# Performance work log

Hardware: AMD Instinct MI355X
Metric: run time of the kernel (lower is better)

## Reference

```python
import jax, jax.numpy as jnp
import numpy as np

L = 8          # number of QTT cores = log2(init_reso)
RESO = 256     # init_reso
MAX_RANK = 256
N_SAMPLES = 4096


def _qtt_ranks(L, max_rank):
    return [min(8 ** k, 8 ** (L - k), max_rank) for k in range(L + 1)]


def setup_inputs() -> dict:
    key = jax.random.key(0)
    ranks = _qtt_ranks(L, MAX_RANK)
    keys = jax.random.split(key, L + 1)
    inp = {}
    for l in range(L):
        shape = (ranks[l], 8, ranks[l + 1])
        scale = (shape[0] * shape[1]) ** -0.5  # keep chain products O(1)
        inp[f"core{l}"] = jax.random.normal(keys[l], shape, dtype=jnp.float32) * scale
    inp["coords_xyz"] = jax.random.randint(keys[L], (N_SAMPLES, 3), 0, RESO)
    return inp


def _coords_to_qtt(coords_xyz, num_cores):
    # coords_xyz: (N, 3) int. Per core l (most-significant bit first):
    # c_l = 4*bit_x + 2*bit_y + bit_z in [0, 8)  -> shape (L, N)
    x, y, z = coords_xyz[:, 0], coords_xyz[:, 1], coords_xyz[:, 2]
    shifts = jnp.arange(num_cores - 1, -1, -1)[:, None]  # (L, 1)
    bx = (x[None, :] >> shifts) & 1
    by = (y[None, :] >> shifts) & 1
    bz = (z[None, :] >> shifts) & 1
    return 4 * bx + 2 * by + bz


def _sample_tt(cores, coords):
    # cores[l]: (r_l, 8, r_{l+1}); coords: (L, N)
    # v starts as first core slice: (N, r_1)  (r_0 == 1)
    v = cores[0][0, coords[0], :]
    for l in range(1, len(cores)):
        # gathered slice: (r_l, N, r_{l+1}) -> (N, r_l, r_{l+1})
        g = jnp.transpose(cores[l][:, coords[l], :], (1, 0, 2))
        v = jnp.einsum('nr,nrs->ns', v, g)
    return v[:, 0]  # r_L == 1 -> (N,)


def reference(core0, core1, core2, core3, core4, core5, core6, core7, coords_xyz):
    cores = [core0, core1, core2, core3, core4, core5, core6, core7]
    coords = _coords_to_qtt(coords_xyz, len(cores))
    return _sample_tt(cores, coords)
```

## Files before the change

### kernel.cpp

```cpp
#include <hip/hip_runtime.h>


typedef unsigned int u32;

__device__ __forceinline__ void async_load16(const float* g, float* l) {
    __builtin_amdgcn_global_load_lds(
        (const __attribute__((address_space(1))) u32*)g,
        (__attribute__((address_space(3))) u32*)l, 16, 0, 0);
}
__device__ __forceinline__ void fma4(float4& c, float a, const float4& b) {
    c.x = fmaf(a, b.x, c.x); c.y = fmaf(a, b.y, c.y);
    c.z = fmaf(a, b.z, c.z); c.w = fmaf(a, b.w, c.w);
}
__device__ __forceinline__ int digit_of(int x, int y, int z, int sh) {
    return 4*((x>>sh)&1) + 2*((y>>sh)&1) + ((z>>sh)&1);
}

__global__ __launch_bounds__(256, 4) void prep_kernel(
    const float* __restrict__ C4, const float* __restrict__ C5,
    const float* __restrict__ C6, const float* __restrict__ C7,
    float* __restrict__ T, float* __restrict__ C4t)
{
    const int t = threadIdx.x;
    const int bx = blockIdx.x;

    if (bx < 64) {
        __shared__ float S6s[8][64];
        const int d5 = bx >> 3, d6 = bx & 7;
#pragma unroll
        for (int j = 0; j < 2; ++j) {
            const int idx = t + 256*j, d7 = idx >> 6, s = idx & 63;
            float acc = 0.f;
#pragma unroll
            for (int jj = 0; jj < 8; ++jj)
                acc = fmaf(C6[s*64 + d6*8 + jj], C7[jj*8 + d7], acc);
            S6s[d7][s] = acc;
        }
        __syncthreads();
        float4 creg[16];
#pragma unroll
        for (int s4 = 0; s4 < 16; ++s4)
            creg[s4] = *(const float4*)(C5 + (size_t)t*512 + d5*64 + s4*4);
#pragma unroll 1
        for (int d7 = 0; d7 < 8; ++d7) {
            float acc = 0.f;
#pragma unroll
            for (int s4 = 0; s4 < 16; ++s4) {
                const float4 a = creg[s4];
                const float4 b = *(const float4*)&S6s[d7][s4*4];
                acc = fmaf(a.x, b.x, acc); acc = fmaf(a.y, b.y, acc);
                acc = fmaf(a.z, b.z, acc); acc = fmaf(a.w, b.w, acc);
            }
            T[(size_t)((d5*8 + d6)*8 + d7)*256 + t] = acc;
        }
    } else {
        const int cb = bx - 64;
        const int d4 = cb >> 2, s5q = cb & 3;
#pragma unroll 8
        for (int j = 0; j < 64; ++j) {
            const int s5 = s5q*64 + j;
            C4t[(size_t)d4*65536 + (size_t)s5*256 + t] =
                C4[(size_t)t*2048 + d4*256 + s5];
        }
    }
}

__device__ __forceinline__ void kgemm16(
    const float* __restrict__ Cd, int rowStride,
    const float (*As)[260], float* BsF,
    float* __restrict__ outP, int rowBase, int mulLo,
    int ln, int wv)
{
    const int kbase = wv * 64;
    float4 acc[16];
#pragma unroll
    for (int r = 0; r < 16; ++r) acc[r] = make_float4(0,0,0,0);

#pragma unroll 1
    for (int s = 0; s < 16; ++s) {
        if (s < 15) {
            const int nb = (s + 1) & 1;
            const int ko = kbase + (s + 1) * 4;
#pragma unroll
            for (int j = 0; j < 4; ++j)
                async_load16(Cd + (size_t)(ko + j)*rowStride + ln*4,
                             BsF + wv*2048 + nb*1024 + j*256 + ln*4);
            asm volatile("s_waitcnt vmcnt(4)" ::: "memory");
        } else {
            asm volatile("s_waitcnt vmcnt(0)" ::: "memory");
        }
        __builtin_amdgcn_sched_barrier(0);
        const int cb = s & 1, kb = kbase + s * 4;
        const float* Bp = BsF + wv*2048 + cb*1024;
        const float4 b0v = *(const float4*)(Bp +   0 + ln*4);
        const float4 b1v = *(const float4*)(Bp + 256 + ln*4);
        const float4 b2v = *(const float4*)(Bp + 512 + ln*4);
        const float4 b3v = *(const float4*)(Bp + 768 + ln*4);
#pragma unroll
        for (int r = 0; r < 16; ++r) {
            const float4 a = *(const float4*)&As[r][kb];
            fma4(acc[r], a.x, b0v); fma4(acc[r], a.y, b1v);
            fma4(acc[r], a.z, b2v); fma4(acc[r], a.w, b3v);
        }
    }

#pragma unroll
    for (int ph = 0; ph < 2; ++ph) {
        float* my = BsF + wv * 2048;
#pragma unroll
        for (int r8 = 0; r8 < 8; ++r8)
            *(float4*)(my + r8*256 + ln*4) = acc[ph*8 + r8];
        __syncthreads();
#pragma unroll
        for (int i = 0; i < 2; ++i) {
            const int rr = wv*2 + i;
            float4 v        = *(const float4*)(BsF +        rr*256 + ln*4);
            const float4 p1 = *(const float4*)(BsF + 2048 + rr*256 + ln*4);
            const float4 p2 = *(const float4*)(BsF + 4096 + rr*256 + ln*4);
            const float4 p3 = *(const float4*)(BsF + 6144 + rr*256 + ln*4);
            v.x += p1.x + p2.x + p3.x; v.y += p1.y + p2.y + p3.y;
            v.z += p1.z + p2.z + p3.z; v.w += p1.w + p2.w + p3.w;
            const int r = ph*8 + rr;
            const int row = rowBase + mulLo*(r & 7) + 8*(r >> 3);
            *(float4*)(outP + (size_t)row*256 + ln*4) = v;
        }
        __syncthreads();
    }
}

__global__ __launch_bounds__(256, 3) void tables_kernel(
    const float* __restrict__ C0, const float* __restrict__ C1,
    const float* __restrict__ C2, const float* __restrict__ C3,
    const float* __restrict__ T, const float* __restrict__ C4t,
    float* __restrict__ P3, float* __restrict__ U)
{
    __shared__ __align__(16) struct {
        float v64[8][64]; float As[16][260]; float Bs[4][2][4][256];
    } u;
    const int t = threadIdx.x;
    const int ln = t & 63, wv = t >> 6;
    const int bx = blockIdx.x;
    float* BsF = &u.Bs[0][0][0][0];
    const int kbase = wv * 64;

    if (bx < 256) {
        const int d3 = bx & 7, d2p = (bx >> 3) & 3, d0 = bx >> 5;
        const float* Cd = C3 + d3 * 256;

#pragma unroll
        for (int j = 0; j < 4; ++j)
            async_load16(Cd + (size_t)(kbase + j)*2048 + ln*4,
                         BsF + wv*2048 + j*256 + ln*4);

#pragma unroll
        for (int j = 0; j < 2; ++j) {
            const int idx = t + 256*j, d1 = idx >> 6, c = idx & 63;
            float acc = 0.f;
#pragma unroll
            for (int r = 0; r < 8; ++r)
                acc = fmaf(C0[d0*8 + r], C1[r*512 + d1*64 + c], acc);
            u.v64[d1][c] = acc;
        }
        __syncthreads();

        {
            const int rbase = wv * 4;
            const int d2 = d2p*2 + (rbase >> 3);
            float4 a0 = make_float4(0,0,0,0), a1 = make_float4(0,0,0,0);
            float4 a2 = make_float4(0,0,0,0), a3 = make_float4(0,0,0,0);
#pragma unroll 8
            for (int j = 0; j < 64; ++j) {
                const float4 c2 = *(const float4*)(C2 + (size_t)j*2048 + d2*256 + ln*4);
                fma4(a0, u.v64[(rbase+0)&7][j], c2);
                fma4(a1, u.v64[(rbase+1)&7][j], c2);
                fma4(a2, u.v64[(rbase+2)&7][j], c2);
                fma4(a3, u.v64[(rbase+3)&7][j], c2);
            }
            *(float4*)&u.As[rbase+0][ln*4] = a0;
            *(float4*)&u.As[rbase+1][ln*4] = a1;
            *(float4*)&u.As[rbase+2][ln*4] = a2;
            *(float4*)&u.As[rbase+3][ln*4] = a3;
        }
        __syncthreads();

        kgemm16(Cd, 2048, u.As, BsF, P3, d0*512 + d2p*16 + d3, 64, ln, wv);
    } else {
        const int ub = bx - 256;
        const int qtile = ub & 31, d4 = ub >> 5;
        const float* Cd = C4t + (size_t)d4*65536;

#pragma unroll
        for (int j = 0; j < 4; ++j)
            async_load16(Cd + (size_t)(kbase + j)*256 + ln*4,
                         BsF + wv*2048 + j*256 + ln*4);
#pragma unroll
        for (int i = 0; i < 4; ++i) {
            const int r = wv*4 + i;
            async_load16(T + (size_t)(qtile*16 + r)*256 + ln*4, &u.As[r][ln*4]);
        }
        __syncthreads();

        kgemm16(Cd, 256, u.As, BsF, U, d4*512 + qtile*16, 1, ln, wv);
    }
}

__global__ __launch_bounds__(256) void final_kernel(
    const float* __restrict__ P3, const float* __restrict__ U,
    const int* __restrict__ coords, int n, float* __restrict__ out)
{
    const int ln = threadIdx.x & 63, wv = threadIdx.x >> 6;
    const int s0 = blockIdx.x * 8 + wv * 2;

    float p[2] = {0.f, 0.f};
    int valid[2];
#pragma unroll
    for (int i = 0; i < 2; ++i) {
        const int s = s0 + i;
        valid[i] = (s < n);
        if (valid[i]) {
            const int x = coords[3*s], y = coords[3*s+1], z = coords[3*s+2];
            const int a  = digit_of(x,y,z,7)*512 + digit_of(x,y,z,6)*64
                         + digit_of(x,y,z,5)*8  + digit_of(x,y,z,4);
            const int d4 = digit_of(x,y,z,3);
            const int q  = digit_of(x,y,z,2)*64 + digit_of(x,y,z,1)*8
                         + digit_of(x,y,z,0);
            const float4 p4 = *(const float4*)(P3 + (size_t)a*256 + ln*4);
            const float4 u4 = *(const float4*)(U + (size_t)(d4*512 + q)*256 + ln*4);
            p[i] = fmaf(p4.x, u4.x, fmaf(p4.y, u4.y,
                   fmaf(p4.z, u4.z, p4.w * u4.w)));
        }
    }
#pragma unroll
    for (int m = 1; m <= 32; m <<= 1) {
        p[0] += __shfl_xor(p[0], m);
        p[1] += __shfl_xor(p[1], m);
    }
    if (ln == 0) {
        if (valid[0]) out[s0]     = p[0];
        if (valid[1]) out[s0 + 1] = p[1];
    }
}

extern "C" void kernel_launch(void* const* d_in, const int* in_sizes, int n_in,
                              void* d_out, int out_size, void* d_ws, size_t ws_size,
                              hipStream_t stream) {
    const float* C0 = (const float*)d_in[0];
    const float* C1 = (const float*)d_in[1];
    const float* C2 = (const float*)d_in[2];
    const float* C3 = (const float*)d_in[3];
    const float* C4 = (const float*)d_in[4];
    const float* C5 = (const float*)d_in[5];
    const float* C6 = (const float*)d_in[6];
    const float* C7 = (const float*)d_in[7];
    const int* coords = (const int*)d_in[8];
    float* out = (float*)d_out;

    const int n = in_sizes[8] / 3;

    float* P3  = (float*)d_ws;
    float* U   = P3  + 4096*256;
    float* Tt  = U   + 4096*256;
    float* C4t = Tt  + 512*256;

    prep_kernel<<<96, 256, 0, stream>>>(C4, C5, C6, C7, Tt, C4t);
    tables_kernel<<<512, 256, 0, stream>>>(C0, C1, C2, C3, Tt, C4t, P3, U);
    final_kernel<<<(n + 7) / 8, 256, 0, stream>>>(P3, U, coords, n, out);
}
```

Before: 113.4 us.

## Split GEMM K-loop per wave over rows, fuse T table build into tables kernel

The old code split the K dimension across four waves, used async global-to-LDS double buffering, and reduced partial sums through shared memory. The new code gives each wave four output rows over the full K range. B operands are loaded directly from global into registers with software prefetch, which removes the cross-wave reduction and its barriers. The C5·C6·C7 table computation moves from the prep kernel into each U-block of tables_kernel, so prep only transposes C4; this recomputes the T tile redundantly per block and lowers the occupancy hint to 2.

```diff
diff --git a/kernel.cpp b/kernel.cpp
--- a/kernel.cpp
+++ b/kernel.cpp
@@ -3,11 +3,6 @@
 
 typedef unsigned int u32;
 
-__device__ __forceinline__ void async_load16(const float* g, float* l) {
-    __builtin_amdgcn_global_load_lds(
-        (const __attribute__((address_space(1))) u32*)g,
-        (__attribute__((address_space(3))) u32*)l, 16, 0, 0);
-}
 __device__ __forceinline__ void fma4(float4& c, float a, const float4& b) {
     c.x = fmaf(a, b.x, c.x); c.y = fmaf(a, b.y, c.y);
     c.z = fmaf(a, b.z, c.z); c.w = fmaf(a, b.w, c.w);
@@ -17,190 +12,179 @@
 }
 
 __global__ __launch_bounds__(256, 4) void prep_kernel(
-    const float* __restrict__ C4, const float* __restrict__ C5,
-    const float* __restrict__ C6, const float* __restrict__ C7,
-    float* __restrict__ T, float* __restrict__ C4t)
+    const float* __restrict__ C4, float* __restrict__ C4t)
 {
     const int t = threadIdx.x;
-    const int bx = blockIdx.x;
-
-    if (bx < 64) {
-        __shared__ float S6s[8][64];
-        const int d5 = bx >> 3, d6 = bx & 7;
-#pragma unroll
-        for (int j = 0; j < 2; ++j) {
-            const int idx = t + 256*j, d7 = idx >> 6, s = idx & 63;
-            float acc = 0.f;
-#pragma unroll
-            for (int jj = 0; jj < 8; ++jj)
-                acc = fmaf(C6[s*64 + d6*8 + jj], C7[jj*8 + d7], acc);
-            S6s[d7][s] = acc;
-        }
-        __syncthreads();
-        float4 creg[16];
-#pragma unroll
-        for (int s4 = 0; s4 < 16; ++s4)
-            creg[s4] = *(const float4*)(C5 + (size_t)t*512 + d5*64 + s4*4);
+    const int cb = blockIdx.x;
+    const int d4 = cb >> 2, s5q = cb & 3;
+#pragma unroll 8
+    for (int j = 0; j < 64; ++j) {
+        const int s5 = s5q*64 + j;
+        C4t[(size_t)d4*65536 + (size_t)s5*256 + t] =
+            C4[(size_t)t*2048 + d4*256 + s5];
+    }
+}
+
+__device__ __forceinline__ void kgemm4(
+    const float* __restrict__ Bg, int rowStride,
+    const float (*As)[260], int r0, int ln,
+    float4& acc0, float4& acc1, float4& acc2, float4& acc3)
+{
+    const float* gp = Bg + ln * 4;
+    float4 bA0 = *(const float4*)(gp + (size_t)0*rowStride);
+    float4 bA1 = *(const float4*)(gp + (size_t)1*rowStride);
+    float4 bA2 = *(const float4*)(gp + (size_t)2*rowStride);
+    float4 bA3 = *(const float4*)(gp + (size_t)3*rowStride);
+    float4 bB0 = *(const float4*)(gp + (size_t)4*rowStride);
+    float4 bB1 = *(const float4*)(gp + (size_t)5*rowStride);
+    float4 bB2 = *(const float4*)(gp + (size_t)6*rowStride);
+    float4 bB3 = *(const float4*)(gp + (size_t)7*rowStride);
+
+#define QTT_COMP(b0, b1, b2, b3, kb)                                   \
+    {   const float4 a0 = *(const float4*)&As[r0+0][(kb)];             \
+        const float4 a1 = *(const float4*)&As[r0+1][(kb)];             \
+        const float4 a2 = *(const float4*)&As[r0+2][(kb)];             \
+        const float4 a3 = *(const float4*)&As[r0+3][(kb)];             \
+        fma4(acc0, a0.x, b0); fma4(acc0, a0.y, b1);                    \
+        fma4(acc0, a0.z, b2); fma4(acc0, a0.w, b3);                    \
+        fma4(acc1, a1.x, b0); fma4(acc1, a1.y, b1);                    \
+        fma4(acc1, a1.z, b2); fma4(acc1, a1.w, b3);                    \
+        fma4(acc2, a2.x, b0); fma4(acc2, a2.y, b1);                    \
+        fma4(acc2, a2.z, b2); fma4(acc2, a2.w, b3);                    \
+        fma4(acc3, a3.x, b0); fma4(acc3, a3.y, b1);                    \
+        fma4(acc3, a3.z, b2); fma4(acc3, a3.w, b3); }
+
 #pragma unroll 1
-        for (int d7 = 0; d7 < 8; ++d7) {
-            float acc = 0.f;
-#pragma unroll
-            for (int s4 = 0; s4 < 16; ++s4) {
-                const float4 a = creg[s4];
-                const float4 b = *(const float4*)&S6s[d7][s4*4];
-                acc = fmaf(a.x, b.x, acc); acc = fmaf(a.y, b.y, acc);
-                acc = fmaf(a.z, b.z, acc); acc = fmaf(a.w, b.w, acc);
-            }
-            T[(size_t)((d5*8 + d6)*8 + d7)*256 + t] = acc;
-        }
-    } else {
-        const int cb = bx - 64;
-        const int d4 = cb >> 2, s5q = cb & 3;
-#pragma unroll 8
-        for (int j = 0; j < 64; ++j) {
-            const int s5 = s5q*64 + j;
-            C4t[(size_t)d4*65536 + (size_t)s5*256 + t] =
-                C4[(size_t)t*2048 + d4*256 + s5];
-        }
-    }
-}
-
-__device__ __forceinline__ void kgemm16(
-    const float* __restrict__ Cd, int rowStride,
-    const float (*As)[260], float* BsF,
-    float* __restrict__ outP, int rowBase, int mulLo,
-    int ln, int wv)
-{
-    const int kbase = wv * 64;
-    float4 acc[16];
-#pragma unroll
-    for (int r = 0; r < 16; ++r) acc[r] = make_float4(0,0,0,0);
-
-#pragma unroll 1
-    for (int s = 0; s < 16; ++s) {
-        if (s < 15) {
-            const int nb = (s + 1) & 1;
-            const int ko = kbase + (s + 1) * 4;
-#pragma unroll
-            for (int j = 0; j < 4; ++j)
-                async_load16(Cd + (size_t)(ko + j)*rowStride + ln*4,
-                             BsF + wv*2048 + nb*1024 + j*256 + ln*4);
-            asm volatile("s_waitcnt vmcnt(4)" ::: "memory");
-        } else {
-            asm volatile("s_waitcnt vmcnt(0)" ::: "memory");
-        }
-        __builtin_amdgcn_sched_barrier(0);
-        const int cb = s & 1, kb = kbase + s * 4;
-        const float* Bp = BsF + wv*2048 + cb*1024;
-        const float4 b0v = *(const float4*)(Bp +   0 + ln*4);
-        const float4 b1v = *(const float4*)(Bp + 256 + ln*4);
-        const float4 b2v = *(const float4*)(Bp + 512 + ln*4);
-        const float4 b3v = *(const float4*)(Bp + 768 + ln*4);
-#pragma unroll
-        for (int r = 0; r < 16; ++r) {
-            const float4 a = *(const float4*)&As[r][kb];
-            fma4(acc[r], a.x, b0v); fma4(acc[r], a.y, b1v);
-            fma4(acc[r], a.z, b2v); fma4(acc[r], a.w, b3v);
-        }
-    }
-
-#pragma unroll
-    for (int ph = 0; ph < 2; ++ph) {
-        float* my = BsF + wv * 2048;
-#pragma unroll
-        for (int r8 = 0; r8 < 8; ++r8)
-            *(float4*)(my + r8*256 + ln*4) = acc[ph*8 + r8];
-        __syncthreads();
-#pragma unroll
-        for (int i = 0; i < 2; ++i) {
-            const int rr = wv*2 + i;
-            float4 v        = *(const float4*)(BsF +        rr*256 + ln*4);
-            const float4 p1 = *(const float4*)(BsF + 2048 + rr*256 + ln*4);
-            const float4 p2 = *(const float4*)(BsF + 4096 + rr*256 + ln*4);
-            const float4 p3 = *(const float4*)(BsF + 6144 + rr*256 + ln*4);
-            v.x += p1.x + p2.x + p3.x; v.y += p1.y + p2.y + p3.y;
-            v.z += p1.z + p2.z + p3.z; v.w += p1.w + p2.w + p3.w;
-            const int r = ph*8 + rr;
-            const int row = rowBase + mulLo*(r & 7) + 8*(r >> 3);
-            *(float4*)(outP + (size_t)row*256 + ln*4) = v;
-        }
-        __syncthreads();
-    }
-}
-
-__global__ __launch_bounds__(256, 3) void tables_kernel(
+    for (int s = 0; s < 32; ++s) {
+        const int k0 = s * 8;
+        QTT_COMP(bA0, bA1, bA2, bA3, k0);
+        if (s < 31) {
+            bA0 = *(const float4*)(gp + (size_t)(k0+ 8)*rowStride);
+            bA1 = *(const float4*)(gp + (size_t)(k0+ 9)*rowStride);
+            bA2 = *(const float4*)(gp + (size_t)(k0+10)*rowStride);
+            bA3 = *(const float4*)(gp + (size_t)(k0+11)*rowStride);
+        }
+        QTT_COMP(bB0, bB1, bB2, bB3, k0 + 4);
+        if (s < 31) {
+            bB0 = *(const float4*)(gp + (size_t)(k0+12)*rowStride);
+            bB1 = *(const float4*)(gp + (size_t)(k0+13)*rowStride);
+            bB2 = *(const float4*)(gp + (size_t)(k0+14)*rowStride);
+            bB3 = *(const float4*)(gp + (size_t)(k0+15)*rowStride);
+        }
+    }
+#undef QTT_COMP
+}
+
+__global__ __launch_bounds__(256, 2) void tables_kernel(
     const float* __restrict__ C0, const float* __restrict__ C1,
     const float* __restrict__ C2, const float* __restrict__ C3,
-    const float* __restrict__ T, const float* __restrict__ C4t,
+    const float* __restrict__ C4t, const float* __restrict__ C5,
+    const float* __restrict__ C6, const float* __restrict__ C7,
     float* __restrict__ P3, float* __restrict__ U)
 {
     __shared__ __align__(16) struct {
-        float v64[8][64]; float As[16][260]; float Bs[4][2][4][256];
+        float small[4][4][64];
+        float As[16][260];
     } u;
     const int t = threadIdx.x;
     const int ln = t & 63, wv = t >> 6;
     const int bx = blockIdx.x;
-    float* BsF = &u.Bs[0][0][0][0];
-    const int kbase = wv * 64;
+
+    float4 acc0 = make_float4(0,0,0,0), acc1 = make_float4(0,0,0,0);
+    float4 acc2 = make_float4(0,0,0,0), acc3 = make_float4(0,0,0,0);
 
     if (bx < 256) {
         const int d3 = bx & 7, d2p = (bx >> 3) & 3, d0 = bx >> 5;
-        const float* Cd = C3 + d3 * 256;
-
-#pragma unroll
-        for (int j = 0; j < 4; ++j)
-            async_load16(Cd + (size_t)(kbase + j)*2048 + ln*4,
-                         BsF + wv*2048 + j*256 + ln*4);
-
-#pragma unroll
-        for (int j = 0; j < 2; ++j) {
-            const int idx = t + 256*j, d1 = idx >> 6, c = idx & 63;
+
+        const int d1base = (wv & 1) * 4;
+#pragma unroll
+        for (int i = 0; i < 4; ++i) {
             float acc = 0.f;
 #pragma unroll
-            for (int r = 0; r < 8; ++r)
-                acc = fmaf(C0[d0*8 + r], C1[r*512 + d1*64 + c], acc);
-            u.v64[d1][c] = acc;
-        }
-        __syncthreads();
-
+            for (int r8 = 0; r8 < 8; ++r8)
+                acc = fmaf(C0[d0*8 + r8],
+                           C1[r8*512 + (d1base + i)*64 + ln], acc);
+            u.small[wv][i][ln] = acc;
+        }
+        __syncthreads();
+
+        const int d2 = d2p*2 + (wv >> 1);
         {
-            const int rbase = wv * 4;
-            const int d2 = d2p*2 + (rbase >> 3);
             float4 a0 = make_float4(0,0,0,0), a1 = make_float4(0,0,0,0);
             float4 a2 = make_float4(0,0,0,0), a3 = make_float4(0,0,0,0);
-#pragma unroll 8
-            for (int j = 0; j < 64; ++j) {
-                const float4 c2 = *(const float4*)(C2 + (size_t)j*2048 + d2*256 + ln*4);
-                fma4(a0, u.v64[(rbase+0)&7][j], c2);
-                fma4(a1, u.v64[(rbase+1)&7][j], c2);
-                fma4(a2, u.v64[(rbase+2)&7][j], c2);
-                fma4(a3, u.v64[(rbase+3)&7][j], c2);
+            const float* c2base = C2 + d2*256 + ln*4;
+#pragma unroll
+            for (int j4 = 0; j4 < 16; ++j4) {
+                const float4 v0 = *(const float4*)&u.small[wv][0][j4*4];
+                const float4 v1 = *(const float4*)&u.small[wv][1][j4*4];
+                const float4 v2 = *(const float4*)&u.small[wv][2][j4*4];
+                const float4 v3 = *(const float4*)&u.small[wv][3][j4*4];
+#define QTT_ASTEP(jj, comp)                                            \
+                { const float4 c2 = *(const float4*)(c2base +          \
+                      (size_t)(j4*4 + jj)*2048);                       \
+                  fma4(a0, v0.comp, c2); fma4(a1, v1.comp, c2);        \
+                  fma4(a2, v2.comp, c2); fma4(a3, v3.comp, c2); }
+                QTT_ASTEP(0, x) QTT_ASTEP(1, y) QTT_ASTEP(2, z) QTT_ASTEP(3, w)
+#undef QTT_ASTEP
             }
-            *(float4*)&u.As[rbase+0][ln*4] = a0;
-            *(float4*)&u.As[rbase+1][ln*4] = a1;
-            *(float4*)&u.As[rbase+2][ln*4] = a2;
-            *(float4*)&u.As[rbase+3][ln*4] = a3;
-        }
-        __syncthreads();
-
-        kgemm16(Cd, 2048, u.As, BsF, P3, d0*512 + d2p*16 + d3, 64, ln, wv);
+            *(float4*)&u.As[wv*4+0][ln*4] = a0;
+            *(float4*)&u.As[wv*4+1][ln*4] = a1;
+            *(float4*)&u.As[wv*4+2][ln*4] = a2;
+            *(float4*)&u.As[wv*4+3][ln*4] = a3;
+        }
+        __syncthreads();
+
+        kgemm4(C3 + d3*256, 2048, u.As, wv*4, ln, acc0, acc1, acc2, acc3);
+
+        const int rb = d0*512 + d2*8 + d3;
+        *(float4*)(P3 + (size_t)(rb + (d1base+0)*64)*256 + ln*4) = acc0;
+        *(float4*)(P3 + (size_t)(rb + (d1base+1)*64)*256 + ln*4) = acc1;
+        *(float4*)(P3 + (size_t)(rb + (d1base+2)*64)*256 + ln*4) = acc2;
+        *(float4*)(P3 + (size_t)(rb + (d1base+3)*64)*256 + ln*4) = acc3;
     } else {
         const int ub = bx - 256;
         const int qtile = ub & 31, d4 = ub >> 5;
-        const float* Cd = C4t + (size_t)d4*65536;
-
-#pragma unroll
-        for (int j = 0; j < 4; ++j)
-            async_load16(Cd + (size_t)(kbase + j)*256 + ln*4,
-                         BsF + wv*2048 + j*256 + ln*4);
+        const int d5 = qtile >> 2;
+
+        float4 creg[16];
+#pragma unroll
+        for (int j4 = 0; j4 < 16; ++j4)
+            creg[j4] = *(const float4*)(C5 + (size_t)t*512 + d5*64 + j4*4);
+
 #pragma unroll
         for (int i = 0; i < 4; ++i) {
             const int r = wv*4 + i;
-            async_load16(T + (size_t)(qtile*16 + r)*256 + ln*4, &u.As[r][ln*4]);
-        }
-        __syncthreads();
-
-        kgemm16(Cd, 256, u.As, BsF, U, d4*512 + qtile*16, 1, ln, wv);
+            const int d6 = (qtile & 3)*2 + (r >> 3), d7 = r & 7;
+            float acc = 0.f;
+#pragma unroll
+            for (int jj = 0; jj < 8; ++jj)
+                acc = fmaf(C6[ln*64 + d6*8 + jj], C7[jj*8 + d7], acc);
+            u.small[wv][i][ln] = acc;
+        }
+        __syncthreads();
+
+#pragma unroll 1
+        for (int r = 0; r < 16; ++r) {
+            float acc = 0.f;
+#pragma unroll
+            for (int j4 = 0; j4 < 16; ++j4) {
+                const float4 s6 = *(const float4*)&u.small[r >> 2][r & 3][j4*4];
+                const float4 c5 = creg[j4];
+                acc = fmaf(c5.x, s6.x, acc); acc = fmaf(c5.y, s6.y, acc);
+                acc = fmaf(c5.z, s6.z, acc); acc = fmaf(c5.w, s6.w, acc);
+            }
+            u.As[r][t] = acc;
+        }
+        __syncthreads();
+
+        kgemm4(C4t + (size_t)d4*65536, 256, u.As, wv*4, ln,
+               acc0, acc1, acc2, acc3);
+
+        const int rb = d4*512 + qtile*16 + wv*4;
+        *(float4*)(U + (size_t)(rb + 0)*256 + ln*4) = acc0;
+        *(float4*)(U + (size_t)(rb + 1)*256 + ln*4) = acc1;
+        *(float4*)(U + (size_t)(rb + 2)*256 + ln*4) = acc2;
+        *(float4*)(U + (size_t)(rb + 3)*256 + ln*4) = acc3;
     }
 }
 
@@ -258,11 +242,11 @@
     const int n = in_sizes[8] / 3;
 
     float* P3  = (float*)d_ws;
-    float* U   = P3  + 4096*256;
-    float* Tt  = U   + 4096*256;
-    float* C4t = Tt  + 512*256;
-
-    prep_kernel<<<96, 256, 0, stream>>>(C4, C5, C6, C7, Tt, C4t);
-    tables_kernel<<<512, 256, 0, stream>>>(C0, C1, C2, C3, Tt, C4t, P3, U);
+    float* U   = P3 + 4096*256;
+    float* C4t = U  + 4096*256;
+
+    prep_kernel<<<32, 256, 0, stream>>>(C4, C4t);
+    tables_kernel<<<512, 256, 0, stream>>>(
+        C0, C1, C2, C3, C4t, C5, C6, C7, P3, U);
     final_kernel<<<(n + 7) / 8, 256, 0, stream>>>(P3, U, coords, n, out);
 }
```

Measured after the change: 115.9 us. 1.02x slower.
